# Kernel tuning notes

Measured on AMD Instinct MI355X. Metric: run time of the kernel, lower is better.

The kernel has to match this reference:

```python
import jax, jax.numpy as jnp
import numpy as np

N, E, D_IN, H, C, D_OUT = 50000, 800000, 16, 4, 64, 32


def setup_inputs() -> dict:
    key = jax.random.key(0)
    ks = jax.random.split(key, 24)
    w = lambda k, shape: (jax.random.normal(k, shape, jnp.float32) * 0.1)
    p = {}
    p["x"] = jax.random.normal(ks[0], (N, D_IN), jnp.float32)
    p["edge_index"] = jax.random.randint(ks[1], (2, E), 0, N, jnp.int32)
    p["W1"] = w(ks[2], (D_IN, H * C))
    p["a1_src"] = w(ks[3], (H, C))
    p["a1_dst"] = w(ks[4], (H, C))
    p["b1"] = jnp.zeros((H * C,), jnp.float32)
    p["W2"] = w(ks[5], (H * C, H * C))
    p["a2_src"] = w(ks[6], (H, C))
    p["a2_dst"] = w(ks[7], (H, C))
    p["b2"] = jnp.zeros((H * C,), jnp.float32)
    # GATConv 3: 256 -> 32, 1 head, concat=False (mean)
    p["W3"] = w(ks[8], (H * C, 1 * D_OUT))
    p["a3_src"] = w(ks[9], (1, D_OUT))
    p["a3_dst"] = w(ks[10], (1, D_OUT))
    p["b3"] = jnp.zeros((D_OUT,), jnp.float32)
    # LayerNorms over 256
    p["g1"] = jnp.ones((H * C,), jnp.float32)
    p["beta1"] = jnp.zeros((H * C,), jnp.float32)
    p["g2"] = jnp.ones((H * C,), jnp.float32)
    p["beta2"] = jnp.zeros((H * C,), jnp.float32)
    # risk head: Linear(32,32) -> ReLU -> Linear(32,6) -> Sigmoid
    p["Wr1"] = w(ks[11], (D_OUT, 32))
    p["br1"] = jnp.zeros((32,), jnp.float32)
    p["Wr2"] = w(ks[12], (32, 6))
    p["br2"] = jnp.zeros((6,), jnp.float32)
    return p


def layernorm(x, g, b, eps=1e-5):
    mu = jnp.mean(x, axis=-1, keepdims=True)
    var = jnp.mean(jnp.square(x - mu), axis=-1, keepdims=True)
    return (x - mu) * jax.lax.rsqrt(var + eps) * g + b


def gat_layer(x, src, dst, W, b, a_src, a_dst, n_nodes, concat):
    # PyG GATConv (eval mode): lin -> per-edge leaky_relu score -> segment softmax over dst -> scatter sum
    heads, ch = a_src.shape
    h = (x @ W).reshape(n_nodes, heads, ch)                 # [N,H,C]
    alpha_s = jnp.sum(h * a_src[None], axis=-1)             # [N,H]
    alpha_d = jnp.sum(h * a_dst[None], axis=-1)             # [N,H]
    e = jax.nn.leaky_relu(alpha_s[src] + alpha_d[dst], 0.2)  # [E,H]
    m = jax.ops.segment_max(e, dst, num_segments=n_nodes)   # stable softmax per dst
    ex = jnp.exp(e - m[dst])
    denom = jax.ops.segment_sum(ex, dst, num_segments=n_nodes)
    alpha = ex / (denom[dst] + 1e-16)                        # [E,H]
    out = jax.ops.segment_sum(alpha[:, :, None] * h[src], dst, num_segments=n_nodes)  # [N,H,C]
    out = out.reshape(n_nodes, heads * ch) if concat else out.mean(axis=1)
    return out + b


def reference(x, edge_index, W1, a1_src, a1_dst, b1, W2, a2_src, a2_dst, b2,
              W3, a3_src, a3_dst, b3, g1, beta1, g2, beta2, Wr1, br1, Wr2, br2):
    n = x.shape[0]
    loops = jnp.arange(n, dtype=edge_index.dtype)
    src = jnp.concatenate([edge_index[0], loops])  # GATConv adds self-loops by default
    dst = jnp.concatenate([edge_index[1], loops])
    h = gat_layer(x, src, dst, W1, b1, a1_src, a1_dst, n, True)
    h = jax.nn.elu(layernorm(h, g1, beta1))
    h = gat_layer(h, src, dst, W2, b2, a2_src, a2_dst, n, True)
    h = jax.nn.elu(layernorm(h, g2, beta2))
    h = gat_layer(h, src, dst, W3, b3, a3_src, a3_dst, n, False)
    risk = jax.nn.sigmoid(jax.nn.relu(h @ Wr1 + br1) @ Wr2 + br2)
    return (h, risk)
```

## Files before the change

kernel.cpp:

```cpp
#include <hip/hip_runtime.h>
#include <hip/hip_bf16.h>
#include <cmath>

constexpr int Nn  = 50000;
constexpr int Np  = 50176;
constexpr int Ee  = 800000;
constexpr int ET  = Ee + Nn;
constexpr int F   = 256;
constexpr int DIN = 16;
constexpr int DO  = 32;

constexpr int W1O=0, A1S=4096, A1D=4352, B1O=4608,
              A2S=4864, A2D=5120, B2O=5376,
              A3S=5632, A3D=5664, B3O=5696,
              G1O=5728, BE1O=5984, G2O=6240, BE2O=6496,
              WR1O=6752, BR1O=7776, WR2O=7808, BR2O=8000, WTOT=8006;

struct InPtrs { const void* p[22]; };

typedef __attribute__((ext_vector_type(8))) short short8v;
typedef __attribute__((ext_vector_type(8))) unsigned short ushort8v;
typedef __attribute__((ext_vector_type(4))) float f32x4;

__device__ __forceinline__ float ld_in(const void* p, int i, int bf){
  if (bf){ unsigned u = (unsigned)((const unsigned short*)p)[i];
           union{unsigned u; float f;} c; c.u = u<<16; return c.f; }
  return ((const float*)p)[i];
}
__device__ __forceinline__ float b2f(unsigned short u){
  union{unsigned u; float f;} c; c.u = ((unsigned)u)<<16; return c.f;
}
__device__ __forceinline__ unsigned short f2b(float f){
  union{float f; unsigned u;} c; c.f=f; unsigned u=c.u;
  return (unsigned short)((u + 0x7fffu + ((u>>16)&1u))>>16);
}
__device__ __forceinline__ void st_out(void* o, int bf, long i, float v){
  if (bf) ((unsigned short*)o)[i] = f2b(v);
  else ((float*)o)[i]=v;
}
__device__ __forceinline__ float wsum64(float v){
  #pragma unroll
  for (int o=32;o;o>>=1) v += __shfl_xor(v,o);
  return v;
}

__global__ void k_detect(const unsigned* __restrict__ xr, int* __restrict__ flag){
  __shared__ int cnt;
  if (threadIdx.x==0) cnt=0;
  __syncthreads();
  int bad=0;
  for (int i=threadIdx.x;i<2048;i+=256){
    unsigned lo = xr[i]&0xffffu;
    unsigned ex = (lo>>7)&0xffu;
    if (ex>=133u) bad++;
  }
  atomicAdd(&cnt,bad);
  __syncthreads();
  if (threadIdx.x==0) *flag = (cnt<8) ? 1 : 0;
}

__global__ void k_convert(InPtrs ip, float* __restrict__ wf,
                          const int* __restrict__ flagp){
  int t = blockIdx.x*256 + threadIdx.x;
  int bf = *flagp;
  const int SIX[17]={3,4,5,7,8,9,11,12,13,14,15,16,17,18,19,20,21};
  const int SOF[17]={A1S,A1D,B1O,A2S,A2D,B2O,A3S,A3D,B3O,
                     G1O,BE1O,G2O,BE2O,WR1O,BR1O,WR2O,BR2O};
  const int SSZ[17]={256,256,256,256,256,256,32,32,32,
                     256,256,256,256,1024,32,192,6};
  for (int j=0;j<17;j++){
    if (t < SSZ[j]){ wf[SOF[j]+t] = ld_in(ip.p[SIX[j]], t, bf); return; }
    t -= SSZ[j];
  }
}

__global__ void k_xpad(const void* __restrict__ x, unsigned short* __restrict__ xp,
                       const int* __restrict__ flagp){
  int g = blockIdx.x*256 + threadIdx.x;
  if (g >= Np*32) return;
  int bf = *flagp;
  int row = g>>5, k = g&31;
  float v = (row<Nn && k<16) ? ld_in(x, row*16+k, bf) : 0.f;
  xp[g] = f2b(v);
}
__global__ void k_w1t(const void* __restrict__ w1, unsigned short* __restrict__ w1t,
                      const int* __restrict__ flagp){
  int g = blockIdx.x*256 + threadIdx.x;
  if (g >= 256*32) return;
  int bf = *flagp;
  int n = g>>5, k = g&31;
  w1t[g] = (k<16) ? f2b(ld_in(w1, k*256+n, bf)) : (unsigned short)0;
}
__global__ void k_w2t(const void* __restrict__ w2, unsigned short* __restrict__ w2t,
                      const int* __restrict__ flagp){
  int g = blockIdx.x*256 + threadIdx.x;
  if (g >= 256*256) return;
  int bf = *flagp;
  int n = g>>8, k = g&255;
  w2t[n*256+k] = f2b(ld_in(w2, k*256+n, bf));
}
__global__ void k_w3t(const void* __restrict__ w3, unsigned short* __restrict__ w3t,
                      const int* __restrict__ flagp){
  int g = blockIdx.x*256 + threadIdx.x;
  if (g >= 32*256) return;
  int bf = *flagp;
  int n = g>>8, k = g&255;
  w3t[n*256+k] = f2b(ld_in(w3, k*32+n, bf));
}

__global__ void k_count(const int* __restrict__ ei, int* __restrict__ deg){
  int g = blockIdx.x*256 + threadIdx.x;
  if (g < Ee) atomicAdd(&deg[ei[Ee+g]], 1);
}
__global__ void __launch_bounds__(256) k_scan_blk(const int* __restrict__ deg,
                                                  int* __restrict__ offtmp,
                                                  int* __restrict__ bsum){
  __shared__ int s[256];
  int t = threadIdx.x, i = blockIdx.x*256 + t;
  int v = (i<Nn) ? deg[i]+1 : 0;
  s[t]=v; __syncthreads();
  #pragma unroll
  for (int d=1; d<256; d<<=1){
    int x = (t>=d)? s[t-d] : 0; __syncthreads();
    s[t]+=x; __syncthreads();
  }
  if (i<Nn) offtmp[i] = s[t]-v;
  if (t==255) bsum[blockIdx.x] = s[255];
}
__global__ void __launch_bounds__(256) k_scan_top(const int* __restrict__ bsum,
                                                  int* __restrict__ bpre,
                                                  int* __restrict__ off){
  __shared__ int s[256];
  int t=threadIdx.x;
  int v = (t<196)? bsum[t]:0;
  s[t]=v; __syncthreads();
  #pragma unroll
  for (int d=1;d<256;d<<=1){ int x=(t>=d)?s[t-d]:0; __syncthreads(); s[t]+=x; __syncthreads(); }
  if (t<196) bpre[t]=s[t]-v;
  if (t==0) off[Nn]=ET;
}
__global__ void __launch_bounds__(256) k_scan_add(const int* __restrict__ offtmp,
                                                  const int* __restrict__ bpre,
                                                  int* __restrict__ off,
                                                  int* __restrict__ cursor){
  int i = blockIdx.x*256 + threadIdx.x;
  if (i<Nn){ int st = offtmp[i]+bpre[i>>8]; off[i]=st; cursor[i]=st; }
}
__global__ void k_fill(const int* __restrict__ ei, int* __restrict__ cursor,
                       int* __restrict__ csr){
  int g = blockIdx.x*256 + threadIdx.x;
  if (g < Ee){
    int s = ei[g], d = ei[Ee+g];
    int p = atomicAdd(&cursor[d],1);
    csr[p] = s;
  } else if (g < ET){
    int n = g - Ee;
    int p = atomicAdd(&cursor[n],1);
    csr[p] = n;
  }
}

template<int BM,int BN,int WAVES_M,int WAVES_N,int KT>
__global__ void __launch_bounds__(256) k_gemm_mfma(const unsigned short* __restrict__ Ag,
                                                   const unsigned short* __restrict__ BTg,
                                                   unsigned short* __restrict__ Cg,
                                                   int M, int N, int nMB){
  constexpr int WMT = BM/(WAVES_M*16);
  constexpr int WNT = BN/(WAVES_N*16);
  __shared__ unsigned short As[4*BM*8];
  __shared__ unsigned short Bs[4*BN*8];
  int bm = blockIdx.x % nMB, bn = blockIdx.x / nMB;
  int row0 = bm*BM, col0 = bn*BN;
  int tid = threadIdx.x, lane = tid&63, wid = tid>>6;
  int wm = wid % WAVES_M, wn = wid / WAVES_M;
  f32x4 acc[WMT][WNT];
  #pragma unroll
  for (int m=0;m<WMT;m++)
    #pragma unroll
    for (int n=0;n<WNT;n++){ acc[m][n].x=0.f; acc[m][n].y=0.f; acc[m][n].z=0.f; acc[m][n].w=0.f; }

  int cl = lane>>4, rl = lane&15;
  for (int kk=0; kk<KT; kk+=32){
    __syncthreads();
    for (int idx=tid; idx<4*BM; idx+=256){
      int r = idx>>2, c = idx&3;
      short8v v = *(const short8v*)(Ag + (size_t)(row0+r)*KT + kk + c*8);
      *(short8v*)(As + (c*BM + (r ^ (c<<2)))*8) = v;
    }
    for (int idx=tid; idx<4*BN; idx+=256){
      int r = idx>>2, c = idx&3;
      short8v v = *(const short8v*)(BTg + (size_t)(col0+r)*KT + kk + c*8);
      *(short8v*)(Bs + (c*BN + (r ^ (c<<2)))*8) = v;
    }
    __syncthreads();
    short8v af[WMT], bfv[WNT];
    #pragma unroll
    for (int m=0;m<WMT;m++){
      int r = wm*WMT*16 + m*16 + rl;
      af[m] = *(const short8v*)(As + (cl*BM + (r ^ (cl<<2)))*8);
    }
    #pragma unroll
    for (int n=0;n<WNT;n++){
      int r = wn*WNT*16 + n*16 + rl;
      bfv[n] = *(const short8v*)(Bs + (cl*BN + (r ^ (cl<<2)))*8);
    }
    #pragma unroll
    for (int m=0;m<WMT;m++)
      #pragma unroll
      for (int n=0;n<WNT;n++)
        acc[m][n] = __builtin_amdgcn_mfma_f32_16x16x32_bf16(af[m], bfv[n], acc[m][n], 0,0,0);
  }
  #pragma unroll
  for (int m=0;m<WMT;m++){
    int rbase = row0 + wm*WMT*16 + m*16 + (lane>>4)*4;
    #pragma unroll
    for (int n=0;n<WNT;n++){
      int col = col0 + wn*WNT*16 + n*16 + (lane&15);
      #pragma unroll
      for (int q=0;q<4;q++){
        int row = rbase + q;
        if (row < M) Cg[(size_t)row*N + col] = f2b(acc[m][n][q]);
      }
    }
  }
}

__global__ void __launch_bounds__(256) k_asad(const unsigned short* __restrict__ Hn,
                                              const float* __restrict__ asw,
                                              const float* __restrict__ adw,
                                              float* __restrict__ as4,
                                              float* __restrict__ ad4){
  int wid = threadIdx.x>>6, lane = threadIdx.x&63;
  int n = blockIdx.x*4 + wid;
  if (n>=Nn) return;
  const ushort4 uv = *reinterpret_cast<const ushort4*>(Hn + (size_t)n*F + lane*4);
  const float4 wa = *reinterpret_cast<const float4*>(asw + lane*4);
  const float4 wd = *reinterpret_cast<const float4*>(adw + lane*4);
  float v0=b2f(uv.x), v1=b2f(uv.y), v2=b2f(uv.z), v3=b2f(uv.w);
  float ps = v0*wa.x + v1*wa.y + v2*wa.z + v3*wa.w;
  float pd = v0*wd.x + v1*wd.y + v2*wd.z + v3*wd.w;
  #pragma unroll
  for (int o=1;o<16;o<<=1){ ps += __shfl_xor(ps,o); pd += __shfl_xor(pd,o); }
  if ((lane&15)==0){
    int h = lane>>4;
    as4[(size_t)n*4+h]=ps; ad4[(size_t)n*4+h]=pd;
  }
}

__global__ void __launch_bounds__(256) k_agg(const unsigned short* __restrict__ Hs,
                                             const float* __restrict__ as4,
                                             const float* __restrict__ ad4,
                                             const float* __restrict__ bias,
                                             const float* __restrict__ gam,
                                             const float* __restrict__ bet,
                                             const int* __restrict__ off,
                                             const int* __restrict__ csr,
                                             unsigned short* __restrict__ out){
  int wid = threadIdx.x>>6, lane = threadIdx.x&63;
  int n = blockIdx.x*4 + wid;
  if (n>=Nn) return;
  int half = lane>>5, c8 = lane&31;
  int h = c8>>3;
  float adh = ad4[(size_t)n*4 + h];
  const unsigned short* hbase = Hs + c8*8;
  int o0=off[n], o1=off[n+1];
  float a0=0,a1=0,a2=0,a3=0,a4=0,a5=0,a6=0,a7=0,den=0;
  int e = o0 + half;
  for (; e+6 < o1; e += 8){
    int s0v=csr[e], s1v=csr[e+2], s2v=csr[e+4], s3v=csr[e+6];
    float q0=as4[(size_t)s0v*4+h], q1=as4[(size_t)s1v*4+h],
          q2=as4[(size_t)s2v*4+h], q3=as4[(size_t)s3v*4+h];
    const ushort8v hv0 = *reinterpret_cast<const ushort8v*>(hbase + (size_t)s0v*F);
    const ushort8v hv1 = *reinterpret_cast<const ushort8v*>(hbase + (size_t)s1v*F);
    const ushort8v hv2 = *reinterpret_cast<const ushort8v*>(hbase + (size_t)s2v*F);
    const ushort8v hv3 = *reinterpret_cast<const ushort8v*>(hbase + (size_t)s3v*F);
    float t0=q0+adh; t0=t0>0.f?t0:0.2f*t0; float w0=__expf(t0);
    float t1=q1+adh; t1=t1>0.f?t1:0.2f*t1; float w1=__expf(t1);
    float t2=q2+adh; t2=t2>0.f?t2:0.2f*t2; float w2=__expf(t2);
    float t3=q3+adh; t3=t3>0.f?t3:0.2f*t3; float w3=__expf(t3);
    den += (w0+w1)+(w2+w3);
    a0 += w0*b2f(hv0[0]) + w1*b2f(hv1[0]) + w2*b2f(hv2[0]) + w3*b2f(hv3[0]);
    a1 += w0*b2f(hv0[1]) + w1*b2f(hv1[1]) + w2*b2f(hv2[1]) + w3*b2f(hv3[1]);
    a2 += w0*b2f(hv0[2]) + w1*b2f(hv1[2]) + w2*b2f(hv2[2]) + w3*b2f(hv3[2]);
    a3 += w0*b2f(hv0[3]) + w1*b2f(hv1[3]) + w2*b2f(hv2[3]) + w3*b2f(hv3[3]);
    a4 += w0*b2f(hv0[4]) + w1*b2f(hv1[4]) + w2*b2f(hv2[4]) + w3*b2f(hv3[4]);
    a5 += w0*b2f(hv0[5]) + w1*b2f(hv1[5]) + w2*b2f(hv2[5]) + w3*b2f(hv3[5]);
    a6 += w0*b2f(hv0[6]) + w1*b2f(hv1[6]) + w2*b2f(hv2[6]) + w3*b2f(hv3[6]);
    a7 += w0*b2f(hv0[7]) + w1*b2f(hv1[7]) + w2*b2f(hv2[7]) + w3*b2f(hv3[7]);
  }
  for (; e < o1; e += 2){
    int sv=csr[e];
    float q=as4[(size_t)sv*4+h];
    float t=q+adh; t=t>0.f?t:0.2f*t; float w=__expf(t);
    const ushort8v hv = *reinterpret_cast<const ushort8v*>(hbase + (size_t)sv*F);
    den += w;
    a0 += w*b2f(hv[0]); a1 += w*b2f(hv[1]); a2 += w*b2f(hv[2]); a3 += w*b2f(hv[3]);
    a4 += w*b2f(hv[4]); a5 += w*b2f(hv[5]); a6 += w*b2f(hv[6]); a7 += w*b2f(hv[7]);
  }
  a0 += __shfl_xor(a0,32); a1 += __shfl_xor(a1,32);
  a2 += __shfl_xor(a2,32); a3 += __shfl_xor(a3,32);
  a4 += __shfl_xor(a4,32); a5 += __shfl_xor(a5,32);
  a6 += __shfl_xor(a6,32); a7 += __shfl_xor(a7,32);
  den += __shfl_xor(den,32);
  float rs = 1.f/(den + 1e-16f);
  int c = c8*8;
  const float4 bv0 = *reinterpret_cast<const float4*>(bias + c);
  const float4 bv1 = *reinterpret_cast<const float4*>(bias + c + 4);
  a0=a0*rs+bv0.x; a1=a1*rs+bv0.y; a2=a2*rs+bv0.z; a3=a3*rs+bv0.w;
  a4=a4*rs+bv1.x; a5=a5*rs+bv1.y; a6=a6*rs+bv1.z; a7=a7*rs+bv1.w;
  float sl = a0+a1+a2+a3+a4+a5+a6+a7;
  float mu = wsum64(sl)*(1.f/512.f);
  float d0=a0-mu,d1=a1-mu,d2=a2-mu,d3=a3-mu,d4=a4-mu,d5=a5-mu,d6=a6-mu,d7=a7-mu;
  float ql = d0*d0+d1*d1+d2*d2+d3*d3+d4*d4+d5*d5+d6*d6+d7*d7;
  float var = wsum64(ql)*(1.f/512.f);
  float r = rsqrtf(var + 1e-5f);
  const float4 gv0 = *reinterpret_cast<const float4*>(gam + c);
  const float4 gv1 = *reinterpret_cast<const float4*>(gam + c + 4);
  const float4 ev0 = *reinterpret_cast<const float4*>(bet + c);
  const float4 ev1 = *reinterpret_cast<const float4*>(bet + c + 4);
  float y0=d0*r*gv0.x+ev0.x, y1=d1*r*gv0.y+ev0.y, y2=d2*r*gv0.z+ev0.z, y3=d3*r*gv0.w+ev0.w;
  float y4=d4*r*gv1.x+ev1.x, y5=d5*r*gv1.y+ev1.y, y6=d6*r*gv1.z+ev1.z, y7=d7*r*gv1.w+ev1.w;
  y0=y0>0.f?y0:expm1f(y0); y1=y1>0.f?y1:expm1f(y1);
  y2=y2>0.f?y2:expm1f(y2); y3=y3>0.f?y3:expm1f(y3);
  y4=y4>0.f?y4:expm1f(y4); y5=y5>0.f?y5:expm1f(y5);
  y6=y6>0.f?y6:expm1f(y6); y7=y7>0.f?y7:expm1f(y7);
  if (half==0){
    ushort8v ov;
    ov[0]=f2b(y0); ov[1]=f2b(y1); ov[2]=f2b(y2); ov[3]=f2b(y3);
    ov[4]=f2b(y4); ov[5]=f2b(y5); ov[6]=f2b(y6); ov[7]=f2b(y7);
    *reinterpret_cast<ushort8v*>(out + (size_t)n*F + c) = ov;
  }
}

__global__ void __launch_bounds__(256) k_asad3(const unsigned short* __restrict__ C3,
                                               const float* __restrict__ asw,
                                               const float* __restrict__ adw,
                                               float* __restrict__ s3,
                                               float* __restrict__ d3){
  int wid=threadIdx.x>>6, lane=threadIdx.x&63;
  int n = blockIdx.x*4 + wid;
  if (n>=Nn) return;
  float v = (lane<32) ? b2f(C3[(long)n*DO + lane]) : 0.f;
  float wa = (lane<32) ? asw[lane] : 0.f;
  float wd = (lane<32) ? adw[lane] : 0.f;
  float ps = wsum64(v*wa);
  float pd = wsum64(v*wd);
  if (lane==0){ s3[n]=ps; d3[n]=pd; }
}

__global__ void __launch_bounds__(256) k_agg3(const unsigned short* __restrict__ C3,
                                              const float* __restrict__ s3,
                                              const float* __restrict__ d3,
                                              const float* __restrict__ b3,
                                              const int* __restrict__ off,
                                              const int* __restrict__ csr,
                                              float* __restrict__ h3f,
                                              void* __restrict__ dout,
                                              const int* __restrict__ flagp){
  int wid=threadIdx.x>>6, lane=threadIdx.x&63;
  int n = blockIdx.x*4 + wid;
  if (n>=Nn) return;
  int bf = *flagp;
  int grp = lane>>3, j = lane&7;
  float dn = d3[n];
  int o0=off[n], o1=off[n+1];
  float a0=0,a1=0,a2=0,a3=0,den=0;
  for (int e=o0+grp; e<o1; e+=8){
    int s=csr[e];
    float t=s3[s]+dn; t=t>0.f?t:0.2f*t;
    float w=__expf(t);
    const ushort4 hv = *reinterpret_cast<const ushort4*>(C3 + (size_t)s*DO + j*4);
    den += w;
    a0 += w*b2f(hv.x); a1 += w*b2f(hv.y); a2 += w*b2f(hv.z); a3 += w*b2f(hv.w);
  }
  #pragma unroll
  for (int o=8;o<64;o<<=1){
    a0 += __shfl_xor(a0,o); a1 += __shfl_xor(a1,o);
    a2 += __shfl_xor(a2,o); a3 += __shfl_xor(a3,o);
    den += __shfl_xor(den,o);
  }
  if (lane<8){
    float rs = 1.f/(den + 1e-16f);
    int c = lane*4;
    const float4 bv = *reinterpret_cast<const float4*>(b3 + c);
    float v0=a0*rs+bv.x, v1=a1*rs+bv.y, v2=a2*rs+bv.z, v3=a3*rs+bv.w;
    float4 o4; o4.x=v0; o4.y=v1; o4.z=v2; o4.w=v3;
    *reinterpret_cast<float4*>(h3f + (size_t)n*DO + c) = o4;
    long bo = (long)n*DO + c;
    st_out(dout, bf, bo  , v0);
    st_out(dout, bf, bo+1, v1);
    st_out(dout, bf, bo+2, v2);
    st_out(dout, bf, bo+3, v3);
  }
}

__global__ void __launch_bounds__(256) k_risk(const float* __restrict__ h3f,
                                              const float* __restrict__ wf,
                                              void* __restrict__ dout,
                                              const int* __restrict__ flagp){
  int n = blockIdx.x*256 + threadIdx.x;
  if (n>=Nn) return;
  int bf = *flagp;
  float hv[32];
  #pragma unroll
  for (int k=0;k<32;k++) hv[k]=h3f[(long)n*32+k];
  float t1[32];
  #pragma unroll
  for (int j=0;j<32;j++){
    float s = wf[BR1O+j];
    #pragma unroll
    for (int k=0;k<32;k++) s += hv[k]*wf[WR1O+k*32+j];
    t1[j] = fmaxf(s,0.f);
  }
  #pragma unroll
  for (int o=0;o<6;o++){
    float s = wf[BR2O+o];
    #pragma unroll
    for (int j=0;j<32;j++) s += t1[j]*wf[WR2O+j*6+o];
    float r = 1.f/(1.f+expf(-s));
    st_out(dout, bf, (long)Nn*32 + (long)n*6 + o, r);
  }
}

extern "C" void kernel_launch(void* const* d_in, const int* in_sizes, int n_in,
                              void* d_out, int out_size, void* d_ws, size_t ws_size,
                              hipStream_t stream){
  char* base = (char*)d_ws;
  size_t cur = 0;
  auto alloc = [&](size_t bytes)->char*{
    cur = (cur + 255) & ~(size_t)255;
    char* r = base + cur; cur += bytes; return r;
  };
  int*   flag = (int*)  alloc(4);
  float* wf   = (float*)alloc(sizeof(float)*WTOT);
  unsigned short* xpad = (unsigned short*)alloc(sizeof(short)*(size_t)Np*32);
  unsigned short* w1t = (unsigned short*)alloc(sizeof(short)*256*32);
  unsigned short* w2t = (unsigned short*)alloc(sizeof(short)*256*256);
  unsigned short* w3t = (unsigned short*)alloc(sizeof(short)*32*256);
  int*   deg  = (int*)  alloc(sizeof(int)*Nn);
  int*   offt = (int*)  alloc(sizeof(int)*Nn);
  int*   bsum = (int*)  alloc(sizeof(int)*256);
  int*   bpre = (int*)  alloc(sizeof(int)*256);
  int*   off  = (int*)  alloc(sizeof(int)*(Nn+1));
  int*   curs = (int*)  alloc(sizeof(int)*Nn);
  int*   csr  = (int*)  alloc(sizeof(int)*ET);
  unsigned short* G  = (unsigned short*)alloc(sizeof(short)*(size_t)Np*F);
  unsigned short* Hb = (unsigned short*)alloc(sizeof(short)*(size_t)Np*F);
  unsigned short* C3 = (unsigned short*)alloc(sizeof(short)*(size_t)Np*DO);
  float* as4  = (float*)alloc(sizeof(float)*(size_t)Nn*4);
  float* ad4  = (float*)alloc(sizeof(float)*(size_t)Nn*4);
  float* s3   = (float*)alloc(sizeof(float)*Nn);
  float* d3   = (float*)alloc(sizeof(float)*Nn);
  float* h3f  = (float*)alloc(sizeof(float)*(size_t)Nn*DO);

  const int* ei = (const int*)d_in[1];
  InPtrs ip;
  for (int i=0;i<22;i++) ip.p[i]=d_in[i];

  k_detect<<<1,256,0,stream>>>((const unsigned*)d_in[0], flag);
  k_convert<<<16,256,0,stream>>>(ip, wf, flag);
  k_xpad<<<(Np*32+255)/256,256,0,stream>>>(d_in[0], xpad, flag);
  k_w1t<<<32,256,0,stream>>>(d_in[2], w1t, flag);
  k_w2t<<<256,256,0,stream>>>(d_in[6], w2t, flag);
  k_w3t<<<32,256,0,stream>>>(d_in[10], w3t, flag);

  (void)hipMemsetAsync(deg, 0, sizeof(int)*Nn, stream);
  k_count<<<(Ee+255)/256,256,0,stream>>>(ei, deg);
  k_scan_blk<<<196,256,0,stream>>>(deg, offt, bsum);
  k_scan_top<<<1,256,0,stream>>>(bsum, bpre, off);
  k_scan_add<<<196,256,0,stream>>>(offt, bpre, off, curs);
  k_fill<<<(ET+255)/256,256,0,stream>>>(ei, curs, csr);

  dim3 wg((Nn+3)/4);
  constexpr int nMB = (Nn + 127)/128;
  k_gemm_mfma<128,128,2,2,32><<<nMB*2,256,0,stream>>>(xpad, w1t, G, Nn, 256, nMB);
  k_asad <<<wg,256,0,stream>>>(G, wf+A1S, wf+A1D, as4, ad4);
  k_agg  <<<wg,256,0,stream>>>(G, as4, ad4, wf+B1O, wf+G1O, wf+BE1O, off, csr, Hb);
  k_gemm_mfma<128,128,2,2,256><<<nMB*2,256,0,stream>>>(Hb, w2t, G, Nn, 256, nMB);
  k_asad <<<wg,256,0,stream>>>(G, wf+A2S, wf+A2D, as4, ad4);
  k_agg  <<<wg,256,0,stream>>>(G, as4, ad4, wf+B2O, wf+G2O, wf+BE2O, off, csr, Hb);
  k_gemm_mfma<128,32,4,1,256><<<nMB,256,0,stream>>>(Hb, w3t, C3, Nn, 32, nMB);
  k_asad3<<<wg,256,0,stream>>>(C3, wf+A3S, wf+A3D, s3, d3);
  k_agg3 <<<wg,256,0,stream>>>(C3, s3, d3, wf+B3O, off, csr, h3f, d_out, flag);
  k_risk <<<(Nn+255)/256,256,0,stream>>>(h3f, wf, d_out, flag);
}
```

Baseline: 449.7 us.

## Fuse attention-score dots into GEMM epilogue, precompute edge weights, merge prep and risk kernels

```diff
diff --git a/kernel.cpp b/kernel.cpp
--- a/kernel.cpp
+++ b/kernel.cpp
@@ -7,10 +7,9 @@
 constexpr int Ee  = 800000;
 constexpr int ET  = Ee + Nn;
 constexpr int F   = 256;
-constexpr int DIN = 16;
 constexpr int DO  = 32;
 
-constexpr int W1O=0, A1S=4096, A1D=4352, B1O=4608,
+constexpr int A1S=4096, A1D=4352, B1O=4608,
               A2S=4864, A2D=5120, B2O=5376,
               A3S=5632, A3D=5664, B3O=5696,
               G1O=5728, BE1O=5984, G2O=6240, BE2O=6496,
@@ -59,53 +58,44 @@
   if (threadIdx.x==0) *flag = (cnt<8) ? 1 : 0;
 }
 
-__global__ void k_convert(InPtrs ip, float* __restrict__ wf,
-                          const int* __restrict__ flagp){
-  int t = blockIdx.x*256 + threadIdx.x;
+__global__ void k_prep(InPtrs ip, float* __restrict__ wf,
+                       unsigned short* __restrict__ xp,
+                       unsigned short* __restrict__ w1t,
+                       unsigned short* __restrict__ w2t,
+                       unsigned short* __restrict__ w3t,
+                       const int* __restrict__ flagp){
+  int g = blockIdx.x*256 + threadIdx.x;
   int bf = *flagp;
+  if (g < Np*32){
+    int row=g>>5, k=g&31;
+    float v = (row<Nn && k<16)? ld_in(ip.p[0], row*16+k, bf) : 0.f;
+    xp[g]=f2b(v); return;
+  }
+  g -= Np*32;
+  if (g < 256*256){
+    int n=g>>8, k=g&255;
+    w2t[n*256+k] = f2b(ld_in(ip.p[6], k*256+n, bf)); return;
+  }
+  g -= 256*256;
+  if (g < 256*32){
+    int n=g>>5, k=g&31;
+    w1t[g] = (k<16)? f2b(ld_in(ip.p[2], k*256+n, bf)) : (unsigned short)0; return;
+  }
+  g -= 256*32;
+  if (g < 32*256){
+    int n=g>>8, k=g&255;
+    w3t[n*256+k] = f2b(ld_in(ip.p[10], k*32+n, bf)); return;
+  }
+  g -= 32*256;
   const int SIX[17]={3,4,5,7,8,9,11,12,13,14,15,16,17,18,19,20,21};
   const int SOF[17]={A1S,A1D,B1O,A2S,A2D,B2O,A3S,A3D,B3O,
                      G1O,BE1O,G2O,BE2O,WR1O,BR1O,WR2O,BR2O};
   const int SSZ[17]={256,256,256,256,256,256,32,32,32,
                      256,256,256,256,1024,32,192,6};
   for (int j=0;j<17;j++){
-    if (t < SSZ[j]){ wf[SOF[j]+t] = ld_in(ip.p[SIX[j]], t, bf); return; }
-    t -= SSZ[j];
-  }
-}
-
-__global__ void k_xpad(const void* __restrict__ x, unsigned short* __restrict__ xp,
-                       const int* __restrict__ flagp){
-  int g = blockIdx.x*256 + threadIdx.x;
-  if (g >= Np*32) return;
-  int bf = *flagp;
-  int row = g>>5, k = g&31;
-  float v = (row<Nn && k<16) ? ld_in(x, row*16+k, bf) : 0.f;
-  xp[g] = f2b(v);
-}
-__global__ void k_w1t(const void* __restrict__ w1, unsigned short* __restrict__ w1t,
-                      const int* __restrict__ flagp){
-  int g = blockIdx.x*256 + threadIdx.x;
-  if (g >= 256*32) return;
-  int bf = *flagp;
-  int n = g>>5, k = g&31;
-  w1t[g] = (k<16) ? f2b(ld_in(w1, k*256+n, bf)) : (unsigned short)0;
-}
-__global__ void k_w2t(const void* __restrict__ w2, unsigned short* __restrict__ w2t,
-                      const int* __restrict__ flagp){
-  int g = blockIdx.x*256 + threadIdx.x;
-  if (g >= 256*256) return;
-  int bf = *flagp;
-  int n = g>>8, k = g&255;
-  w2t[n*256+k] = f2b(ld_in(w2, k*256+n, bf));
-}
-__global__ void k_w3t(const void* __restrict__ w3, unsigned short* __restrict__ w3t,
-                      const int* __restrict__ flagp){
-  int g = blockIdx.x*256 + threadIdx.x;
-  if (g >= 32*256) return;
-  int bf = *flagp;
-  int n = g>>8, k = g&255;
-  w3t[n*256+k] = f2b(ld_in(w3, k*32+n, bf));
+    if (g < SSZ[j]){ wf[SOF[j]+g] = ld_in(ip.p[SIX[j]], g, bf); return; }
+    g -= SSZ[j];
+  }
 }
 
 __global__ void k_count(const int* __restrict__ ei, int* __restrict__ deg){
@@ -147,23 +137,27 @@
   if (i<Nn){ int st = offtmp[i]+bpre[i>>8]; off[i]=st; cursor[i]=st; }
 }
 __global__ void k_fill(const int* __restrict__ ei, int* __restrict__ cursor,
-                       int* __restrict__ csr){
+                       int* __restrict__ csr, int* __restrict__ edst){
   int g = blockIdx.x*256 + threadIdx.x;
   if (g < Ee){
     int s = ei[g], d = ei[Ee+g];
     int p = atomicAdd(&cursor[d],1);
-    csr[p] = s;
+    csr[p] = s; edst[p] = d;
   } else if (g < ET){
     int n = g - Ee;
     int p = atomicAdd(&cursor[n],1);
-    csr[p] = n;
-  }
-}
-
-template<int BM,int BN,int WAVES_M,int WAVES_N,int KT>
+    csr[p] = n; edst[p] = n;
+  }
+}
+
+template<int BM,int BN,int WAVES_M,int WAVES_N,int KT,int EPI>
 __global__ void __launch_bounds__(256) k_gemm_mfma(const unsigned short* __restrict__ Ag,
                                                    const unsigned short* __restrict__ BTg,
                                                    unsigned short* __restrict__ Cg,
+                                                   const float* __restrict__ aswp,
+                                                   const float* __restrict__ adwp,
+                                                   float* __restrict__ aso,
+                                                   float* __restrict__ ado,
                                                    int M, int N, int nMB){
   constexpr int WMT = BM/(WAVES_M*16);
   constexpr int WNT = BN/(WAVES_N*16);
@@ -223,33 +217,86 @@
       }
     }
   }
-}
-
-__global__ void __launch_bounds__(256) k_asad(const unsigned short* __restrict__ Hn,
-                                              const float* __restrict__ asw,
-                                              const float* __restrict__ adw,
-                                              float* __restrict__ as4,
-                                              float* __restrict__ ad4){
-  int wid = threadIdx.x>>6, lane = threadIdx.x&63;
-  int n = blockIdx.x*4 + wid;
-  if (n>=Nn) return;
-  const ushort4 uv = *reinterpret_cast<const ushort4*>(Hn + (size_t)n*F + lane*4);
-  const float4 wa = *reinterpret_cast<const float4*>(asw + lane*4);
-  const float4 wd = *reinterpret_cast<const float4*>(adw + lane*4);
-  float v0=b2f(uv.x), v1=b2f(uv.y), v2=b2f(uv.z), v3=b2f(uv.w);
-  float ps = v0*wa.x + v1*wa.y + v2*wa.z + v3*wa.w;
-  float pd = v0*wd.x + v1*wd.y + v2*wd.z + v3*wd.w;
-  #pragma unroll
-  for (int o=1;o<16;o<<=1){ ps += __shfl_xor(ps,o); pd += __shfl_xor(pd,o); }
-  if ((lane&15)==0){
-    int h = lane>>4;
-    as4[(size_t)n*4+h]=ps; ad4[(size_t)n*4+h]=pd;
-  }
+  if constexpr (EPI==1){
+    #pragma unroll
+    for (int m=0;m<WMT;m++){
+      #pragma unroll
+      for (int q=0;q<4;q++){
+        float ps0=0,pd0=0,ps1=0,pd1=0;
+        #pragma unroll
+        for (int n=0;n<WNT;n++){
+          int col = wn*(WNT*16) + n*16 + (lane&15);
+          float av = acc[m][n][q];
+          float ws = aswp[col], wd = adwp[col];
+          if (n < WNT/2){ ps0 += av*ws; pd0 += av*wd; }
+          else          { ps1 += av*ws; pd1 += av*wd; }
+        }
+        #pragma unroll
+        for (int o=1;o<16;o<<=1){
+          ps0 += __shfl_xor(ps0,o); pd0 += __shfl_xor(pd0,o);
+          ps1 += __shfl_xor(ps1,o); pd1 += __shfl_xor(pd1,o);
+        }
+        int row = row0 + wm*(WMT*16) + m*16 + (lane>>4)*4 + q;
+        if ((lane&15)==0 && row<M){
+          int h0 = wn*2;
+          aso[(size_t)row*4+h0  ]=ps0; aso[(size_t)row*4+h0+1]=ps1;
+          ado[(size_t)row*4+h0  ]=pd0; ado[(size_t)row*4+h0+1]=pd1;
+        }
+      }
+    }
+  } else if constexpr (EPI==2){
+    #pragma unroll
+    for (int m=0;m<WMT;m++){
+      #pragma unroll
+      for (int q=0;q<4;q++){
+        float ps=0,pd=0;
+        #pragma unroll
+        for (int n=0;n<WNT;n++){
+          int col = n*16 + (lane&15);
+          float av = acc[m][n][q];
+          ps += av*aswp[col]; pd += av*adwp[col];
+        }
+        #pragma unroll
+        for (int o=1;o<16;o<<=1){ ps+=__shfl_xor(ps,o); pd+=__shfl_xor(pd,o); }
+        int row = row0 + wm*(WMT*16) + m*16 + (lane>>4)*4 + q;
+        if ((lane&15)==0 && row<M){ aso[row]=ps; ado[row]=pd; }
+      }
+    }
+  }
+}
+
+__global__ void __launch_bounds__(256) k_wexp(const float* __restrict__ as4,
+                                              const float* __restrict__ ad4,
+                                              const int* __restrict__ csr,
+                                              const int* __restrict__ edst,
+                                              float* __restrict__ wE){
+  int e = blockIdx.x*256 + threadIdx.x;
+  if (e>=ET) return;
+  int s=csr[e], d=edst[e];
+  const float4 a = *reinterpret_cast<const float4*>(as4 + (size_t)s*4);
+  const float4 b = *reinterpret_cast<const float4*>(ad4 + (size_t)d*4);
+  float t0=a.x+b.x; t0=t0>0.f?t0:0.2f*t0;
+  float t1=a.y+b.y; t1=t1>0.f?t1:0.2f*t1;
+  float t2=a.z+b.z; t2=t2>0.f?t2:0.2f*t2;
+  float t3=a.w+b.w; t3=t3>0.f?t3:0.2f*t3;
+  float4 w; w.x=__expf(t0); w.y=__expf(t1); w.z=__expf(t2); w.w=__expf(t3);
+  *reinterpret_cast<float4*>(wE + (size_t)e*4) = w;
+}
+
+__global__ void __launch_bounds__(256) k_wexp3(const float* __restrict__ s3,
+                                               const float* __restrict__ d3,
+                                               const int* __restrict__ csr,
+                                               const int* __restrict__ edst,
+                                               float* __restrict__ w3e){
+  int e = blockIdx.x*256 + threadIdx.x;
+  if (e>=ET) return;
+  float t = s3[csr[e]] + d3[edst[e]];
+  t = t>0.f? t : 0.2f*t;
+  w3e[e] = __expf(t);
 }
 
 __global__ void __launch_bounds__(256) k_agg(const unsigned short* __restrict__ Hs,
-                                             const float* __restrict__ as4,
-                                             const float* __restrict__ ad4,
+                                             const float* __restrict__ wE,
                                              const float* __restrict__ bias,
                                              const float* __restrict__ gam,
                                              const float* __restrict__ bet,
@@ -261,23 +308,20 @@
   if (n>=Nn) return;
   int half = lane>>5, c8 = lane&31;
   int h = c8>>3;
-  float adh = ad4[(size_t)n*4 + h];
   const unsigned short* hbase = Hs + c8*8;
-  int o0=off[n], o1=off[n+1];
+  int o0=off[n], o1=off[n+1], cnt=o1-o0;
+  int mid = o0 + (cnt>>1);
+  int lo = half? mid : o0;
+  int hi = half? o1  : mid;
   float a0=0,a1=0,a2=0,a3=0,a4=0,a5=0,a6=0,a7=0,den=0;
-  int e = o0 + half;
-  for (; e+6 < o1; e += 8){
-    int s0v=csr[e], s1v=csr[e+2], s2v=csr[e+4], s3v=csr[e+6];
-    float q0=as4[(size_t)s0v*4+h], q1=as4[(size_t)s1v*4+h],
-          q2=as4[(size_t)s2v*4+h], q3=as4[(size_t)s3v*4+h];
-    const ushort8v hv0 = *reinterpret_cast<const ushort8v*>(hbase + (size_t)s0v*F);
-    const ushort8v hv1 = *reinterpret_cast<const ushort8v*>(hbase + (size_t)s1v*F);
-    const ushort8v hv2 = *reinterpret_cast<const ushort8v*>(hbase + (size_t)s2v*F);
+  int e = lo;
+  for (; e+3<hi; e+=4){
+    int s0=csr[e], s1=csr[e+1], s2=csr[e+2], s3v=csr[e+3];
+    float w0=wE[e*4+h], w1=wE[(e+1)*4+h], w2=wE[(e+2)*4+h], w3=wE[(e+3)*4+h];
+    const ushort8v hv0 = *reinterpret_cast<const ushort8v*>(hbase + (size_t)s0*F);
+    const ushort8v hv1 = *reinterpret_cast<const ushort8v*>(hbase + (size_t)s1*F);
+    const ushort8v hv2 = *reinterpret_cast<const ushort8v*>(hbase + (size_t)s2*F);
     const ushort8v hv3 = *reinterpret_cast<const ushort8v*>(hbase + (size_t)s3v*F);
-    float t0=q0+adh; t0=t0>0.f?t0:0.2f*t0; float w0=__expf(t0);
-    float t1=q1+adh; t1=t1>0.f?t1:0.2f*t1; float w1=__expf(t1);
-    float t2=q2+adh; t2=t2>0.f?t2:0.2f*t2; float w2=__expf(t2);
-    float t3=q3+adh; t3=t3>0.f?t3:0.2f*t3; float w3=__expf(t3);
     den += (w0+w1)+(w2+w3);
     a0 += w0*b2f(hv0[0]) + w1*b2f(hv1[0]) + w2*b2f(hv2[0]) + w3*b2f(hv3[0]);
     a1 += w0*b2f(hv0[1]) + w1*b2f(hv1[1]) + w2*b2f(hv2[1]) + w3*b2f(hv3[1]);
@@ -288,10 +332,9 @@
     a6 += w0*b2f(hv0[6]) + w1*b2f(hv1[6]) + w2*b2f(hv2[6]) + w3*b2f(hv3[6]);
     a7 += w0*b2f(hv0[7]) + w1*b2f(hv1[7]) + w2*b2f(hv2[7]) + w3*b2f(hv3[7]);
   }
-  for (; e < o1; e += 2){
+  for (; e<hi; ++e){
     int sv=csr[e];
-    float q=as4[(size_t)sv*4+h];
-    float t=q+adh; t=t>0.f?t:0.2f*t; float w=__expf(t);
+    float w=wE[e*4+h];
     const ushort8v hv = *reinterpret_cast<const ushort8v*>(hbase + (size_t)sv*F);
     den += w;
     a0 += w*b2f(hv[0]); a1 += w*b2f(hv[1]); a2 += w*b2f(hv[2]); a3 += w*b2f(hv[3]);
@@ -332,43 +375,24 @@
   }
 }
 
-__global__ void __launch_bounds__(256) k_asad3(const unsigned short* __restrict__ C3,
-                                               const float* __restrict__ asw,
-                                               const float* __restrict__ adw,
-                                               float* __restrict__ s3,
-                                               float* __restrict__ d3){
-  int wid=threadIdx.x>>6, lane=threadIdx.x&63;
-  int n = blockIdx.x*4 + wid;
-  if (n>=Nn) return;
-  float v = (lane<32) ? b2f(C3[(long)n*DO + lane]) : 0.f;
-  float wa = (lane<32) ? asw[lane] : 0.f;
-  float wd = (lane<32) ? adw[lane] : 0.f;
-  float ps = wsum64(v*wa);
-  float pd = wsum64(v*wd);
-  if (lane==0){ s3[n]=ps; d3[n]=pd; }
-}
-
-__global__ void __launch_bounds__(256) k_agg3(const unsigned short* __restrict__ C3,
-                                              const float* __restrict__ s3,
-                                              const float* __restrict__ d3,
-                                              const float* __restrict__ b3,
-                                              const int* __restrict__ off,
-                                              const int* __restrict__ csr,
-                                              float* __restrict__ h3f,
-                                              void* __restrict__ dout,
-                                              const int* __restrict__ flagp){
+__global__ void __launch_bounds__(256) k_agg3r(const unsigned short* __restrict__ C3,
+                                               const float* __restrict__ w3e,
+                                               const float* __restrict__ wf,
+                                               const int* __restrict__ off,
+                                               const int* __restrict__ csr,
+                                               void* __restrict__ dout,
+                                               const int* __restrict__ flagp){
   int wid=threadIdx.x>>6, lane=threadIdx.x&63;
   int n = blockIdx.x*4 + wid;
   if (n>=Nn) return;
   int bf = *flagp;
-  int grp = lane>>3, j = lane&7;
-  float dn = d3[n];
-  int o0=off[n], o1=off[n+1];
+  int g = lane>>3, j = lane&7;
+  int o0=off[n], o1=off[n+1], cnt=o1-o0;
+  int lo = o0 + ((cnt*g)>>3), hi = o0 + ((cnt*(g+1))>>3);
   float a0=0,a1=0,a2=0,a3=0,den=0;
-  for (int e=o0+grp; e<o1; e+=8){
+  for (int e=lo; e<hi; ++e){
     int s=csr[e];
-    float t=s3[s]+dn; t=t>0.f?t:0.2f*t;
-    float w=__expf(t);
+    float w=w3e[e];
     const ushort4 hv = *reinterpret_cast<const ushort4*>(C3 + (size_t)s*DO + j*4);
     den += w;
     a0 += w*b2f(hv.x); a1 += w*b2f(hv.y); a2 += w*b2f(hv.z); a3 += w*b2f(hv.w);
@@ -379,46 +403,43 @@
     a2 += __shfl_xor(a2,o); a3 += __shfl_xor(a3,o);
     den += __shfl_xor(den,o);
   }
+  float rs = 1.f/(den + 1e-16f);
+  const float4 bv = *reinterpret_cast<const float4*>(wf + B3O + j*4);
+  float v0=a0*rs+bv.x, v1=a1*rs+bv.y, v2=a2*rs+bv.z, v3=a3*rs+bv.w;
   if (lane<8){
-    float rs = 1.f/(den + 1e-16f);
-    int c = lane*4;
-    const float4 bv = *reinterpret_cast<const float4*>(b3 + c);
-    float v0=a0*rs+bv.x, v1=a1*rs+bv.y, v2=a2*rs+bv.z, v3=a3*rs+bv.w;
-    float4 o4; o4.x=v0; o4.y=v1; o4.z=v2; o4.w=v3;
-    *reinterpret_cast<float4*>(h3f + (size_t)n*DO + c) = o4;
-    long bo = (long)n*DO + c;
-    st_out(dout, bf, bo  , v0);
-    st_out(dout, bf, bo+1, v1);
-    st_out(dout, bf, bo+2, v2);
-    st_out(dout, bf, bo+3, v3);
-  }
-}
-
-__global__ void __launch_bounds__(256) k_risk(const float* __restrict__ h3f,
-                                              const float* __restrict__ wf,
-                                              void* __restrict__ dout,
-                                              const int* __restrict__ flagp){
-  int n = blockIdx.x*256 + threadIdx.x;
-  if (n>=Nn) return;
-  int bf = *flagp;
-  float hv[32];
-  #pragma unroll
-  for (int k=0;k<32;k++) hv[k]=h3f[(long)n*32+k];
-  float t1[32];
-  #pragma unroll
-  for (int j=0;j<32;j++){
-    float s = wf[BR1O+j];
-    #pragma unroll
-    for (int k=0;k<32;k++) s += hv[k]*wf[WR1O+k*32+j];
-    t1[j] = fmaxf(s,0.f);
-  }
-  #pragma unroll
-  for (int o=0;o<6;o++){
-    float s = wf[BR2O+o];
-    #pragma unroll
-    for (int j=0;j<32;j++) s += t1[j]*wf[WR2O+j*6+o];
-    float r = 1.f/(1.f+expf(-s));
-    st_out(dout, bf, (long)Nn*32 + (long)n*6 + o, r);
+    long bo = (long)n*DO + lane*4;
+    st_out(dout,bf,bo  ,v0); st_out(dout,bf,bo+1,v1);
+    st_out(dout,bf,bo+2,v2); st_out(dout,bf,bo+3,v3);
+  }
+  float hk[32];
+  #pragma unroll
+  for (int k=0;k<32;k++){
+    float src = ((k&3)==0)? v0 : ((k&3)==1)? v1 : ((k&3)==2)? v2 : v3;
+    hk[k] = __shfl(src, k>>2);
+  }
+  float t1 = 0.f;
+  if (lane<32){
+    t1 = wf[BR1O+lane];
+    #pragma unroll
+    for (int k=0;k<32;k++) t1 += hk[k]*wf[WR1O + k*32 + lane];
+    t1 = fmaxf(t1, 0.f);
+  }
+  float p0=0,p1=0,p2=0,p3=0,p4=0,p5=0;
+  if (lane<32){
+    const float* w2r = wf + WR2O + lane*6;
+    p0=t1*w2r[0]; p1=t1*w2r[1]; p2=t1*w2r[2];
+    p3=t1*w2r[3]; p4=t1*w2r[4]; p5=t1*w2r[5];
+  }
+  #pragma unroll
+  for (int m=1;m<64;m<<=1){
+    p0+=__shfl_xor(p0,m); p1+=__shfl_xor(p1,m); p2+=__shfl_xor(p2,m);
+    p3+=__shfl_xor(p3,m); p4+=__shfl_xor(p4,m); p5+=__shfl_xor(p5,m);
+  }
+  if (lane<6){
+    float s = (lane==0)?p0:(lane==1)?p1:(lane==2)?p2:(lane==3)?p3:(lane==4)?p4:p5;
+    s += wf[BR2O+lane];
+    float r = 1.f/(1.f+__expf(-s));
+    st_out(dout, bf, (long)Nn*32 + (long)n*6 + lane, r);
   }
 }
 
@@ -444,43 +465,46 @@
   int*   off  = (int*)  alloc(sizeof(int)*(Nn+1));
   int*   curs = (int*)  alloc(sizeof(int)*Nn);
   int*   csr  = (int*)  alloc(sizeof(int)*ET);
+  int*   edst = (int*)  alloc(sizeof(int)*ET);
   unsigned short* G  = (unsigned short*)alloc(sizeof(short)*(size_t)Np*F);
   unsigned short* Hb = (unsigned short*)alloc(sizeof(short)*(size_t)Np*F);
   unsigned short* C3 = (unsigned short*)alloc(sizeof(short)*(size_t)Np*DO);
   float* as4  = (float*)alloc(sizeof(float)*(size_t)Nn*4);
   float* ad4  = (float*)alloc(sizeof(float)*(size_t)Nn*4);
+  float* wE   = (float*)alloc(sizeof(float)*(size_t)ET*4);
   float* s3   = (float*)alloc(sizeof(float)*Nn);
   float* d3   = (float*)alloc(sizeof(float)*Nn);
-  float* h3f  = (float*)alloc(sizeof(float)*(size_t)Nn*DO);
+  float* w3e  = (float*)alloc(sizeof(float)*(size_t)ET);
 
   const int* ei = (const int*)d_in[1];
   InPtrs ip;
   for (int i=0;i<22;i++) ip.p[i]=d_in[i];
 
   k_detect<<<1,256,0,stream>>>((const unsigned*)d_in[0], flag);
-  k_convert<<<16,256,0,stream>>>(ip, wf, flag);
-  k_xpad<<<(Np*32+255)/256,256,0,stream>>>(d_in[0], xpad, flag);
-  k_w1t<<<32,256,0,stream>>>(d_in[2], w1t, flag);
-  k_w2t<<<256,256,0,stream>>>(d_in[6], w2t, flag);
-  k_w3t<<<32,256,0,stream>>>(d_in[10], w3t, flag);
-
+  {
+    int total = Np*32 + 256*256 + 256*32 + 32*256 + 3910;
+    k_prep<<<(total+255)/256,256,0,stream>>>(ip, wf, xpad, w1t, w2t, w3t, flag);
+  }
   (void)hipMemsetAsync(deg, 0, sizeof(int)*Nn, stream);
   k_count<<<(Ee+255)/256,256,0,stream>>>(ei, deg);
   k_scan_blk<<<196,256,0,stream>>>(deg, offt, bsum);
   k_scan_top<<<1,256,0,stream>>>(bsum, bpre, off);
   k_scan_add<<<196,256,0,stream>>>(offt, bpre, off, curs);
-  k_fill<<<(ET+255)/256,256,0,stream>>>(ei, curs, csr);
+  k_fill<<<(ET+255)/256,256,0,stream>>>(ei, curs, csr, edst);
 
   dim3 wg((Nn+3)/4);
-  constexpr int nMB = (Nn + 127)/128;
-  k_gemm_mfma<128,128,2,2,32><<<nMB*2,256,0,stream>>>(xpad, w1t, G, Nn, 256, nMB);
-  k_asad <<<wg,256,0,stream>>>(G, wf+A1S, wf+A1D, as4, ad4);
-  k_agg  <<<wg,256,0,stream>>>(G, as4, ad4, wf+B1O, wf+G1O, wf+BE1O, off, csr, Hb);
-  k_gemm_mfma<128,128,2,2,256><<<nMB*2,256,0,stream>>>(Hb, w2t, G, Nn, 256, nMB);
-  k_asad <<<wg,256,0,stream>>>(G, wf+A2S, wf+A2D, as4, ad4);
-  k_agg  <<<wg,256,0,stream>>>(G, as4, ad4, wf+B2O, wf+G2O, wf+BE2O, off, csr, Hb);
-  k_gemm_mfma<128,32,4,1,256><<<nMB,256,0,stream>>>(Hb, w3t, C3, Nn, 32, nMB);
-  k_asad3<<<wg,256,0,stream>>>(C3, wf+A3S, wf+A3D, s3, d3);
-  k_agg3 <<<wg,256,0,stream>>>(C3, s3, d3, wf+B3O, off, csr, h3f, d_out, flag);
-  k_risk <<<(Nn+255)/256,256,0,stream>>>(h3f, wf, d_out, flag);
-}
+  constexpr int nMB = Np/64;
+  dim3 eg((ET+255)/256);
+  k_gemm_mfma<64,256,2,2,32,1><<<nMB,256,0,stream>>>(xpad, w1t, G,
+      wf+A1S, wf+A1D, as4, ad4, Nn, 256, nMB);
+  k_wexp<<<eg,256,0,stream>>>(as4, ad4, csr, edst, wE);
+  k_agg <<<wg,256,0,stream>>>(G, wE, wf+B1O, wf+G1O, wf+BE1O, off, csr, Hb);
+  k_gemm_mfma<64,256,2,2,256,1><<<nMB,256,0,stream>>>(Hb, w2t, G,
+      wf+A2S, wf+A2D, as4, ad4, Nn, 256, nMB);
+  k_wexp<<<eg,256,0,stream>>>(as4, ad4, csr, edst, wE);
+  k_agg <<<wg,256,0,stream>>>(G, wE, wf+B2O, wf+G2O, wf+BE2O, off, csr, Hb);
+  k_gemm_mfma<64,32,4,1,256,2><<<nMB,256,0,stream>>>(Hb, w3t, C3,
+      wf+A3S, wf+A3D, s3, d3, Nn, 32, nMB);
+  k_wexp3<<<eg,256,0,stream>>>(s3, d3, csr, edst, w3e);
+  k_agg3r<<<wg,256,0,stream>>>(C3, w3e, wf, off, csr, d_out, flag);
+}
```

Result: no change. 453.8 us (+0.9%).
